# Kernel optimization log

Measured on AMD Instinct MI355X. Metric: run time of the kernel, lower is better.

## Reference

```python
import jax, jax.numpy as jnp
import numpy as np

TEMPERATURE = 0.5
EPS = 1e-12  # matches torch F.normalize clamp_min


def setup_inputs() -> dict:
    key = jax.random.key(0)
    k1, k2 = jax.random.split(key)
    N, D, C = 8192, 128, 64
    out_1 = jax.random.normal(k1, (N, D), dtype=jnp.float32)
    label = jax.random.randint(k2, (N,), 0, C, dtype=jnp.int64)
    return {"out_1": out_1, "label": label}


def reference(out_1, label):
    N = out_1.shape[0]
    # L2 normalize rows (F.normalize with eps clamp)
    norm = jnp.maximum(jnp.linalg.norm(out_1, axis=-1, keepdims=True), EPS)
    x = out_1 / norm
    # exp-scaled cosine similarity matrix [N, N]
    sim = jnp.exp(jnp.matmul(x, x.T) / TEMPERATURE)
    not_diag = 1.0 - jnp.eye(N, dtype=sim.dtype)
    # negatives: all off-diagonal entries per row
    negative_sim = jnp.sum(sim * not_diag, axis=-1)
    # positives: same label, excluding self; mean per row
    pos_mask = (label[:, None] == label[None, :]).astype(sim.dtype) * not_diag
    pos_count = jnp.sum(pos_mask, axis=-1)
    pos_sim = jnp.sum(sim * pos_mask, axis=-1) / pos_count
    return jnp.mean(-jnp.log(pos_sim / negative_sim))
```

## Files before the change

### kernel.cpp

```cpp
#include <hip/hip_runtime.h>
#include <hip/hip_bf16.h>
#include <stdint.h>

typedef __attribute__((ext_vector_type(8))) __bf16 bf16x8;
typedef __attribute__((ext_vector_type(16))) float floatx16;

#if __has_builtin(__builtin_amdgcn_exp2f)
#define EXP2F(x) __builtin_amdgcn_exp2f(x)
#else
#define EXP2F(x) exp2f(x)
#endif

#define GAS __attribute__((address_space(1)))
#define LAS __attribute__((address_space(3)))

#define SCALE_SQRT 1.69864359f

__global__ __launch_bounds__(256) void k_prep(const float* __restrict__ x,
                                              const int* __restrict__ raw,
                                              ushort* __restrict__ xb,
                                              int* __restrict__ lab, int N) {
  const int row = (blockIdx.x * 256 + threadIdx.x) >> 6;
  const int lane = threadIdx.x & 63;
  if (row >= N) return;
  const int probe = raw[2 * lane + 1];
  const bool is64 = (__ballot(probe != 0) == 0ull);
  const float2 v = ((const float2*)(x + (size_t)row * 128))[lane];
  float ss = v.x * v.x + v.y * v.y;
#pragma unroll
  for (int m = 1; m < 64; m <<= 1) ss += __shfl_xor(ss, m, 64);
  const float rn = SCALE_SQRT / fmaxf(sqrtf(ss), 1e-12f);
  __hip_bfloat162 o;
  o.x = __float2bfloat16(v.x * rn);
  o.y = __float2bfloat16(v.y * rn);
  ((__hip_bfloat162*)xb)[row * 64 + lane] = o;
  if (lane == 0) lab[row] = is64 ? raw[2 * row] : raw[row];
}

__global__ __launch_bounds__(256, 2) void k_sim(const ushort* __restrict__ xb,
                                                const int* __restrict__ lab,
                                                float* __restrict__ pneg,
                                                float* __restrict__ ppos,
                                                int N) {
  __shared__ ushort ldsB[128 * 128];
  __shared__ float cb[4 * 2 * 2 * 2 * 32];
  const int tid = threadIdx.x;
  const int lane = tid & 63;
  const int wv = tid >> 6;
  const int l31 = lane & 31, g2 = lane >> 5;
  const int l15 = lane & 15, g4 = lane >> 4;

  const int bid = blockIdx.x;
  int u = (int)((sqrtf(8.0f * (float)bid + 1.0f) - 1.0f) * 0.5f);
  while ((u + 1) * (u + 2) / 2 <= bid) ++u;
  while (u * (u + 1) / 2 > bid) --u;
  const int s = bid - u * (u + 1) / 2;
  const int i0 = s * 128;
  const int jb0 = u * 128;

#pragma unroll
  for (int it = 0; it < 8; ++it) {
    const int r0 = it * 16 + wv * 4;
    const int lr = r0 + g4;
    const int kb = l15 ^ (lr & 15);
    const ushort* gp = xb + (size_t)(jb0 + lr) * 128 + kb * 8;
    __builtin_amdgcn_global_load_lds((GAS void*)gp, (LAS void*)&ldsB[r0 * 128], 16, 0, 0);
  }

  const int arow = i0 + wv * 32 + l31;
  bf16x8 af[8];
#pragma unroll
  for (int kt = 0; kt < 8; ++kt)
    af[kt] = *(const bf16x8*)(xb + (size_t)arow * 128 + (kt * 2 + g2) * 8);

  int liw[4];
#pragma unroll
  for (int q = 0; q < 4; ++q) {
    const int rb = i0 + wv * 32 + 8 * q + 4 * g2;
    liw[q] = (lab[rb] & 255) | ((lab[rb + 1] & 255) << 8) |
             ((lab[rb + 2] & 255) << 16) | ((lab[rb + 3] & 255) << 24);
  }
  int lj[4];
#pragma unroll
  for (int t = 0; t < 2; ++t)
#pragma unroll
    for (int h = 0; h < 2; ++h) lj[t * 2 + h] = lab[jb0 + t * 64 + h * 32 + l31];

  floatx16 vneg = (floatx16)(0.0f), vpos = (floatx16)(0.0f);
  const bool offd = (u != s);
  __syncthreads();

#pragma unroll
  for (int tile = 0; tile < 2; ++tile) {
    floatx16 acc0 = (floatx16)(0.0f), acc1 = (floatx16)(0.0f);
#pragma unroll
    for (int kt = 0; kt < 8; ++kt) {
      const int br0 = tile * 64 + l31;
      const int br1 = tile * 64 + 32 + l31;
      const bf16x8 b0 = *(const bf16x8*)&ldsB[br0 * 128 + (((kt * 2 + g2) ^ (br0 & 15)) * 8)];
      const bf16x8 b1 = *(const bf16x8*)&ldsB[br1 * 128 + (((kt * 2 + g2) ^ (br1 & 15)) * 8)];
      acc0 = __builtin_amdgcn_mfma_f32_32x32x16_bf16(af[kt], b0, acc0, 0, 0, 0);
      acc1 = __builtin_amdgcn_mfma_f32_32x32x16_bf16(af[kt], b1, acc1, 0, 0, 0);
    }

    if (offd) {
      float cn0 = 0.0f, cn1 = 0.0f, cp0 = 0.0f, cp1 = 0.0f;
#pragma unroll
      for (int r = 0; r < 16; ++r) {
        const int lr = (liw[r >> 2] >> ((r & 3) * 8)) & 255;
        const float e0 = EXP2F(acc0[r]);
        const float e1 = EXP2F(acc1[r]);
        const float s0 = (lr == lj[tile * 2 + 0]) ? e0 : 0.0f;
        const float s1 = (lr == lj[tile * 2 + 1]) ? e1 : 0.0f;
        vneg[r] += e0 + e1;
        vpos[r] += s0 + s1;
        cn0 += e0; cp0 += s0;
        cn1 += e1; cp1 += s1;
      }
      {
        float a0 = cn0 + __shfl_xor(cn0, 32, 64);
        float b0 = cp0 + __shfl_xor(cp0, 32, 64);
        float a1 = cn1 + __shfl_xor(cn1, 32, 64);
        float b1 = cp1 + __shfl_xor(cp1, 32, 64);
        if (lane < 32) {
          cb[(((wv * 2 + tile) * 2 + 0) * 2 + 0) * 32 + l31] = a0;
          cb[(((wv * 2 + tile) * 2 + 0) * 2 + 1) * 32 + l31] = b0;
          cb[(((wv * 2 + tile) * 2 + 1) * 2 + 0) * 32 + l31] = a1;
          cb[(((wv * 2 + tile) * 2 + 1) * 2 + 1) * 32 + l31] = b1;
        }
      }
    } else {
      const int jc0 = tile * 64 + l31;
      const int jc1 = tile * 64 + 32 + l31;
#pragma unroll
      for (int r = 0; r < 16; ++r) {
        const int lr = (liw[r >> 2] >> ((r & 3) * 8)) & 255;
        const int ir = wv * 32 + (r & 3) + 8 * (r >> 2) + 4 * g2;
        float e0 = EXP2F(acc0[r]);
        float e1 = EXP2F(acc1[r]);
        if (ir == jc0) e0 = 0.0f;
        if (ir == jc1) e1 = 0.0f;
        vneg[r] += e0 + e1;
        vpos[r] += ((lr == lj[tile * 2 + 0]) ? e0 : 0.0f) +
                   ((lr == lj[tile * 2 + 1]) ? e1 : 0.0f);
      }
    }
  }

#pragma unroll
  for (int r = 0; r < 16; ++r) {
    float n = vneg[r], p = vpos[r];
#pragma unroll
    for (int m = 1; m < 32; m <<= 1) {
      n += __shfl_xor(n, m, 64);
      p += __shfl_xor(p, m, 64);
    }
    if (l31 == 0) {
      const int row = i0 + wv * 32 + (r & 3) + 8 * (r >> 2) + 4 * g2;
      pneg[(size_t)u * N + row] = n;
      ppos[(size_t)u * N + row] = p;
    }
  }

  if (offd) {
    __syncthreads();
    const int c5 = tid & 31;
    const int np = (tid >> 5) & 1;
    const int h = (tid >> 6) & 1;
    const int t = (tid >> 7) & 1;
    float v = 0.0f;
#pragma unroll
    for (int w = 0; w < 4; ++w)
      v += cb[(((w * 2 + t) * 2 + h) * 2 + np) * 32 + c5];
    const int jrow = jb0 + t * 64 + h * 32 + c5;
    if (np == 0) pneg[(size_t)s * N + jrow] = v;
    else         ppos[(size_t)s * N + jrow] = v;
  }
}

__global__ __launch_bounds__(256) void k_final(const float* __restrict__ pneg,
                                               const float* __restrict__ ppos,
                                               const int* __restrict__ lab,
                                               double* __restrict__ partial,
                                               int N, int nstrip) {
  __shared__ int h[64];
  __shared__ double wsum[4];
  const int tid = threadIdx.x;
  if (tid < 64) h[tid] = 0;
  __syncthreads();
  for (int i = tid; i < N; i += 256) atomicAdd(&h[lab[i] & 63], 1);
  __syncthreads();
  const int r = blockIdx.x * 256 + tid;
  double v = 0.0;
  if (r < N) {
    float n = 0.0f, p = 0.0f;
#pragma unroll 8
    for (int cc = 0; cc < nstrip; ++cc) {
      n += pneg[(size_t)cc * N + r];
      p += ppos[(size_t)cc * N + r];
    }
    const float cnt = (float)(h[lab[r] & 63] - 1);
    v = (double)logf(n * cnt / p);
  }
#pragma unroll
  for (int m = 1; m < 64; m <<= 1) v += __shfl_xor(v, m, 64);
  if ((tid & 63) == 0) wsum[tid >> 6] = v;
  __syncthreads();
  if (tid == 0) partial[blockIdx.x] = wsum[0] + wsum[1] + wsum[2] + wsum[3];
}

__global__ __launch_bounds__(64) void k_write(const double* __restrict__ partial,
                                              float* __restrict__ out, int nfb, int N) {
  const int l = threadIdx.x;
  double v = 0.0;
  for (int i = l; i < nfb; i += 64) v += partial[i];
#pragma unroll
  for (int m = 1; m < 64; m <<= 1) v += __shfl_xor(v, m, 64);
  if (l == 0) out[0] = (float)(v / (double)N);
}

extern "C" void kernel_launch(void* const* d_in, const int* in_sizes, int n_in,
                              void* d_out, int out_size, void* d_ws, size_t ws_size,
                              hipStream_t stream) {
  const float* x = (const float*)d_in[0];
  const int* raw_label = (const int*)d_in[1];
  const int N = in_sizes[1];
  const int nstrip = N / 128;
  char* ws = (char*)d_ws;
  ushort* xb = (ushort*)ws;
  float* pneg = (float*)(ws + (size_t)N * 128 * 2);
  float* ppos = pneg + (size_t)nstrip * N;
  int* lab = (int*)(ppos + (size_t)nstrip * N);
  double* partial = (double*)(lab + N);
  float* out = (float*)d_out;

  const int pairs = nstrip * (nstrip + 1) / 2;
  const int nfb = (N + 255) / 256;

  k_prep<<<dim3(N / 4), dim3(256), 0, stream>>>(x, raw_label, xb, lab, N);
  k_sim<<<dim3(pairs), dim3(256), 0, stream>>>(xb, lab, pneg, ppos, N);
  k_final<<<dim3(nfb), dim3(256), 0, stream>>>(pneg, ppos, lab, partial, N, nstrip);
  k_write<<<dim3(1), dim3(64), 0, stream>>>(partial, out, nfb, N);
}
```

Before: 99.65 us.

## Make k_sim persistent over tile pairs with double-buffered LDS prefetch

The similarity kernel now launches a fixed grid of 512 blocks, each walking 4–5 consecutive triangular tile pairs. The next B tile is prefetched into a second LDS buffer while the current one is computed, and column partial sums are deferred into a double-buffered cb array. This hides the global-to-LDS load latency and cuts per-block launch and prologue cost. Labels are stored as bytes and neg/pos partials are packed as float2, which trims memory traffic. The grid size and pair split are hardcoded for N=8192 (2080 pairs = 32*5 + 480*4), and doubling LDS use may limit occupancy.

```diff
diff --git a/kernel.cpp b/kernel.cpp
--- a/kernel.cpp
+++ b/kernel.cpp
@@ -19,7 +19,8 @@
 __global__ __launch_bounds__(256) void k_prep(const float* __restrict__ x,
                                               const int* __restrict__ raw,
                                               ushort* __restrict__ xb,
-                                              int* __restrict__ lab, int N) {
+                                              unsigned char* __restrict__ lab8,
+                                              int N) {
   const int row = (blockIdx.x * 256 + threadIdx.x) >> 6;
   const int lane = threadIdx.x & 63;
   if (row >= N) return;
@@ -34,153 +35,181 @@
   o.x = __float2bfloat16(v.x * rn);
   o.y = __float2bfloat16(v.y * rn);
   ((__hip_bfloat162*)xb)[row * 64 + lane] = o;
-  if (lane == 0) lab[row] = is64 ? raw[2 * row] : raw[row];
+  if (lane == 0) lab8[row] = (unsigned char)(is64 ? raw[2 * row] : raw[row]);
 }
 
 __global__ __launch_bounds__(256, 2) void k_sim(const ushort* __restrict__ xb,
-                                                const int* __restrict__ lab,
-                                                float* __restrict__ pneg,
-                                                float* __restrict__ ppos,
+                                                const unsigned char* __restrict__ lab8,
+                                                float2* __restrict__ ppart,
                                                 int N) {
-  __shared__ ushort ldsB[128 * 128];
-  __shared__ float cb[4 * 2 * 2 * 2 * 32];
+  __shared__ ushort ldsB[2][128 * 128];
+  __shared__ float cb[2][4 * 2 * 2 * 2 * 32];
   const int tid = threadIdx.x;
   const int lane = tid & 63;
   const int wv = tid >> 6;
   const int l31 = lane & 31, g2 = lane >> 5;
   const int l15 = lane & 15, g4 = lane >> 4;
 
-  const int bid = blockIdx.x;
-  int u = (int)((sqrtf(8.0f * (float)bid + 1.0f) - 1.0f) * 0.5f);
-  while ((u + 1) * (u + 2) / 2 <= bid) ++u;
-  while (u * (u + 1) / 2 > bid) --u;
-  const int s = bid - u * (u + 1) / 2;
-  const int i0 = s * 128;
-  const int jb0 = u * 128;
-
-#pragma unroll
-  for (int it = 0; it < 8; ++it) {
-    const int r0 = it * 16 + wv * 4;
-    const int lr = r0 + g4;
-    const int kb = l15 ^ (lr & 15);
-    const ushort* gp = xb + (size_t)(jb0 + lr) * 128 + kb * 8;
-    __builtin_amdgcn_global_load_lds((GAS void*)gp, (LAS void*)&ldsB[r0 * 128], 16, 0, 0);
-  }
-
-  const int arow = i0 + wv * 32 + l31;
-  bf16x8 af[8];
-#pragma unroll
-  for (int kt = 0; kt < 8; ++kt)
-    af[kt] = *(const bf16x8*)(xb + (size_t)arow * 128 + (kt * 2 + g2) * 8);
-
-  int liw[4];
-#pragma unroll
-  for (int q = 0; q < 4; ++q) {
-    const int rb = i0 + wv * 32 + 8 * q + 4 * g2;
-    liw[q] = (lab[rb] & 255) | ((lab[rb + 1] & 255) << 8) |
-             ((lab[rb + 2] & 255) << 16) | ((lab[rb + 3] & 255) << 24);
-  }
-  int lj[4];
-#pragma unroll
-  for (int t = 0; t < 2; ++t)
-#pragma unroll
-    for (int h = 0; h < 2; ++h) lj[t * 2 + h] = lab[jb0 + t * 64 + h * 32 + l31];
-
-  floatx16 vneg = (floatx16)(0.0f), vpos = (floatx16)(0.0f);
-  const bool offd = (u != s);
-  __syncthreads();
-
-#pragma unroll
-  for (int tile = 0; tile < 2; ++tile) {
-    floatx16 acc0 = (floatx16)(0.0f), acc1 = (floatx16)(0.0f);
-#pragma unroll
-    for (int kt = 0; kt < 8; ++kt) {
-      const int br0 = tile * 64 + l31;
-      const int br1 = tile * 64 + 32 + l31;
-      const bf16x8 b0 = *(const bf16x8*)&ldsB[br0 * 128 + (((kt * 2 + g2) ^ (br0 & 15)) * 8)];
-      const bf16x8 b1 = *(const bf16x8*)&ldsB[br1 * 128 + (((kt * 2 + g2) ^ (br1 & 15)) * 8)];
-      acc0 = __builtin_amdgcn_mfma_f32_32x32x16_bf16(af[kt], b0, acc0, 0, 0, 0);
-      acc1 = __builtin_amdgcn_mfma_f32_32x32x16_bf16(af[kt], b1, acc1, 0, 0, 0);
-    }
-
-    if (offd) {
-      float cn0 = 0.0f, cn1 = 0.0f, cp0 = 0.0f, cp1 = 0.0f;
-#pragma unroll
-      for (int r = 0; r < 16; ++r) {
-        const int lr = (liw[r >> 2] >> ((r & 3) * 8)) & 255;
-        const float e0 = EXP2F(acc0[r]);
-        const float e1 = EXP2F(acc1[r]);
-        const float s0 = (lr == lj[tile * 2 + 0]) ? e0 : 0.0f;
-        const float s1 = (lr == lj[tile * 2 + 1]) ? e1 : 0.0f;
-        vneg[r] += e0 + e1;
-        vpos[r] += s0 + s1;
-        cn0 += e0; cp0 += s0;
-        cn1 += e1; cp1 += s1;
-      }
-      {
+  const int b = blockIdx.x;
+  const int p0 = b * 4 + (b < 32 ? b : 32);
+  const int np = (b < 32) ? 5 : 4;
+
+  int u = (int)((sqrtf(8.0f * (float)p0 + 1.0f) - 1.0f) * 0.5f);
+  while ((u + 1) * (u + 2) / 2 <= p0) ++u;
+  while (u * (u + 1) / 2 > p0) --u;
+  int s = p0 - u * (u + 1) / 2;
+
+  auto stageB = [&](int buf, int uu) {
+    const int jb = uu * 128;
+#pragma unroll
+    for (int it = 0; it < 8; ++it) {
+      const int r0 = it * 16 + wv * 4;
+      const int lr = r0 + g4;
+      const int kb = l15 ^ (lr & 15);
+      const ushort* gp = xb + (size_t)(jb + lr) * 128 + kb * 8;
+      __builtin_amdgcn_global_load_lds((GAS void*)gp, (LAS void*)&ldsB[buf][r0 * 128], 16, 0, 0);
+    }
+  };
+
+  stageB(0, u);
+  asm volatile("s_waitcnt vmcnt(0)" ::: "memory");
+  __builtin_amdgcn_s_barrier();
+  __builtin_amdgcn_sched_barrier(0);
+
+  int ps = 0, pu = 0;
+  bool poffd = false;
+  const uint* lab32 = (const uint*)lab8;
+
+  for (int k = 0; k < np; ++k) {
+    const int cur = k & 1;
+    const int i0 = s * 128, jb0 = u * 128;
+    const bool offd = (s != u);
+
+    if (k > 0 && poffd && tid < 128) {
+      const int t = (tid >> 6) & 1, h = (tid >> 5) & 1, c5 = tid & 31;
+      float n = 0.0f, p = 0.0f;
+#pragma unroll
+      for (int w = 0; w < 4; ++w) {
+        n += cb[cur ^ 1][(((w * 2 + t) * 2 + h) * 2 + 0) * 32 + c5];
+        p += cb[cur ^ 1][(((w * 2 + t) * 2 + h) * 2 + 1) * 32 + c5];
+      }
+      const int jrow = pu * 128 + t * 64 + h * 32 + c5;
+      ppart[(size_t)ps * N + jrow] = float2{n, p};
+    }
+
+    const int arow = i0 + wv * 32 + l31;
+    bf16x8 af[8];
+#pragma unroll
+    for (int kt = 0; kt < 8; ++kt)
+      af[kt] = *(const bf16x8*)(xb + (size_t)arow * 128 + (kt * 2 + g2) * 8);
+    uint liw[4];
+#pragma unroll
+    for (int q = 0; q < 4; ++q)
+      liw[q] = lab32[(i0 + wv * 32 + 8 * q + 4 * g2) >> 2];
+    int lj[4];
+#pragma unroll
+    for (int t = 0; t < 2; ++t)
+#pragma unroll
+      for (int h = 0; h < 2; ++h) lj[t * 2 + h] = lab8[jb0 + t * 64 + h * 32 + l31];
+
+    int ns = s + 1, nu = u;
+    if (ns > nu) { ns = 0; ++nu; }
+    if (k + 1 < np) stageB(cur ^ 1, nu);
+
+    floatx16 vneg = (floatx16)(0.0f), vpos = (floatx16)(0.0f);
+#pragma unroll
+    for (int tile = 0; tile < 2; ++tile) {
+      floatx16 acc0 = (floatx16)(0.0f), acc1 = (floatx16)(0.0f);
+#pragma unroll
+      for (int kt = 0; kt < 8; ++kt) {
+        const int br0 = tile * 64 + l31;
+        const int br1 = tile * 64 + 32 + l31;
+        const bf16x8 b0 = *(const bf16x8*)&ldsB[cur][br0 * 128 + (((kt * 2 + g2) ^ (br0 & 15)) * 8)];
+        const bf16x8 b1 = *(const bf16x8*)&ldsB[cur][br1 * 128 + (((kt * 2 + g2) ^ (br1 & 15)) * 8)];
+        acc0 = __builtin_amdgcn_mfma_f32_32x32x16_bf16(af[kt], b0, acc0, 0, 0, 0);
+        acc1 = __builtin_amdgcn_mfma_f32_32x32x16_bf16(af[kt], b1, acc1, 0, 0, 0);
+      }
+      if (offd) {
+        float cn0 = 0.0f, cn1 = 0.0f, cp0 = 0.0f, cp1 = 0.0f;
+#pragma unroll
+        for (int r = 0; r < 16; ++r) {
+          const int lr = (liw[r >> 2] >> ((r & 3) * 8)) & 255;
+          const float e0 = EXP2F(acc0[r]);
+          const float e1 = EXP2F(acc1[r]);
+          const float s0 = (lr == lj[tile * 2 + 0]) ? e0 : 0.0f;
+          const float s1 = (lr == lj[tile * 2 + 1]) ? e1 : 0.0f;
+          vneg[r] += e0 + e1;
+          vpos[r] += s0 + s1;
+          cn0 += e0; cp0 += s0;
+          cn1 += e1; cp1 += s1;
+        }
         float a0 = cn0 + __shfl_xor(cn0, 32, 64);
         float b0 = cp0 + __shfl_xor(cp0, 32, 64);
         float a1 = cn1 + __shfl_xor(cn1, 32, 64);
         float b1 = cp1 + __shfl_xor(cp1, 32, 64);
         if (lane < 32) {
-          cb[(((wv * 2 + tile) * 2 + 0) * 2 + 0) * 32 + l31] = a0;
-          cb[(((wv * 2 + tile) * 2 + 0) * 2 + 1) * 32 + l31] = b0;
-          cb[(((wv * 2 + tile) * 2 + 1) * 2 + 0) * 32 + l31] = a1;
-          cb[(((wv * 2 + tile) * 2 + 1) * 2 + 1) * 32 + l31] = b1;
+          cb[cur][(((wv * 2 + tile) * 2 + 0) * 2 + 0) * 32 + l31] = a0;
+          cb[cur][(((wv * 2 + tile) * 2 + 0) * 2 + 1) * 32 + l31] = b0;
+          cb[cur][(((wv * 2 + tile) * 2 + 1) * 2 + 0) * 32 + l31] = a1;
+          cb[cur][(((wv * 2 + tile) * 2 + 1) * 2 + 1) * 32 + l31] = b1;
         }
-      }
-    } else {
-      const int jc0 = tile * 64 + l31;
-      const int jc1 = tile * 64 + 32 + l31;
-#pragma unroll
-      for (int r = 0; r < 16; ++r) {
-        const int lr = (liw[r >> 2] >> ((r & 3) * 8)) & 255;
-        const int ir = wv * 32 + (r & 3) + 8 * (r >> 2) + 4 * g2;
-        float e0 = EXP2F(acc0[r]);
-        float e1 = EXP2F(acc1[r]);
-        if (ir == jc0) e0 = 0.0f;
-        if (ir == jc1) e1 = 0.0f;
-        vneg[r] += e0 + e1;
-        vpos[r] += ((lr == lj[tile * 2 + 0]) ? e0 : 0.0f) +
-                   ((lr == lj[tile * 2 + 1]) ? e1 : 0.0f);
-      }
-    }
+      } else {
+        const int jc0 = tile * 64 + l31;
+        const int jc1 = tile * 64 + 32 + l31;
+#pragma unroll
+        for (int r = 0; r < 16; ++r) {
+          const int lr = (liw[r >> 2] >> ((r & 3) * 8)) & 255;
+          const int ir = wv * 32 + (r & 3) + 8 * (r >> 2) + 4 * g2;
+          float e0 = EXP2F(acc0[r]);
+          float e1 = EXP2F(acc1[r]);
+          if (ir == jc0) e0 = 0.0f;
+          if (ir == jc1) e1 = 0.0f;
+          vneg[r] += e0 + e1;
+          vpos[r] += ((lr == lj[tile * 2 + 0]) ? e0 : 0.0f) +
+                     ((lr == lj[tile * 2 + 1]) ? e1 : 0.0f);
+        }
+      }
+    }
+
+#pragma unroll
+    for (int r = 0; r < 16; ++r) {
+      float n = vneg[r], p = vpos[r];
+#pragma unroll
+      for (int m = 1; m < 32; m <<= 1) {
+        n += __shfl_xor(n, m, 64);
+        p += __shfl_xor(p, m, 64);
+      }
+      if (l31 == 0) {
+        const int row = i0 + wv * 32 + (r & 3) + 8 * (r >> 2) + 4 * g2;
+        ppart[(size_t)u * N + row] = float2{n, p};
+      }
+    }
+
+    asm volatile("s_waitcnt vmcnt(16) lgkmcnt(0)" ::: "memory");
+    __builtin_amdgcn_s_barrier();
+    __builtin_amdgcn_sched_barrier(0);
+
+    ps = s; pu = u; poffd = offd;
+    s = ns; u = nu;
   }
 
-#pragma unroll
-  for (int r = 0; r < 16; ++r) {
-    float n = vneg[r], p = vpos[r];
-#pragma unroll
-    for (int m = 1; m < 32; m <<= 1) {
-      n += __shfl_xor(n, m, 64);
-      p += __shfl_xor(p, m, 64);
-    }
-    if (l31 == 0) {
-      const int row = i0 + wv * 32 + (r & 3) + 8 * (r >> 2) + 4 * g2;
-      pneg[(size_t)u * N + row] = n;
-      ppos[(size_t)u * N + row] = p;
-    }
+  __syncthreads();
+  if (poffd && tid < 128) {
+    const int last = (np - 1) & 1;
+    const int t = (tid >> 6) & 1, h = (tid >> 5) & 1, c5 = tid & 31;
+    float n = 0.0f, p = 0.0f;
+#pragma unroll
+    for (int w = 0; w < 4; ++w) {
+      n += cb[last][(((w * 2 + t) * 2 + h) * 2 + 0) * 32 + c5];
+      p += cb[last][(((w * 2 + t) * 2 + h) * 2 + 1) * 32 + c5];
+    }
+    const int jrow = pu * 128 + t * 64 + h * 32 + c5;
+    ppart[(size_t)ps * N + jrow] = float2{n, p};
   }
-
-  if (offd) {
-    __syncthreads();
-    const int c5 = tid & 31;
-    const int np = (tid >> 5) & 1;
-    const int h = (tid >> 6) & 1;
-    const int t = (tid >> 7) & 1;
-    float v = 0.0f;
-#pragma unroll
-    for (int w = 0; w < 4; ++w)
-      v += cb[(((w * 2 + t) * 2 + h) * 2 + np) * 32 + c5];
-    const int jrow = jb0 + t * 64 + h * 32 + c5;
-    if (np == 0) pneg[(size_t)s * N + jrow] = v;
-    else         ppos[(size_t)s * N + jrow] = v;
-  }
-}
-
-__global__ __launch_bounds__(256) void k_final(const float* __restrict__ pneg,
-                                               const float* __restrict__ ppos,
-                                               const int* __restrict__ lab,
+}
+
+__global__ __launch_bounds__(256) void k_final(const float2* __restrict__ ppart,
+                                               const unsigned char* __restrict__ lab8,
                                                double* __restrict__ partial,
                                                int N, int nstrip) {
   __shared__ int h[64];
@@ -188,7 +217,7 @@
   const int tid = threadIdx.x;
   if (tid < 64) h[tid] = 0;
   __syncthreads();
-  for (int i = tid; i < N; i += 256) atomicAdd(&h[lab[i] & 63], 1);
+  for (int i = tid; i < N; i += 256) atomicAdd(&h[lab8[i] & 63], 1);
   __syncthreads();
   const int r = blockIdx.x * 256 + tid;
   double v = 0.0;
@@ -196,10 +225,11 @@
     float n = 0.0f, p = 0.0f;
 #pragma unroll 8
     for (int cc = 0; cc < nstrip; ++cc) {
-      n += pneg[(size_t)cc * N + r];
-      p += ppos[(size_t)cc * N + r];
-    }
-    const float cnt = (float)(h[lab[r] & 63] - 1);
+      const float2 w = ppart[(size_t)cc * N + r];
+      n += w.x;
+      p += w.y;
+    }
+    const float cnt = (float)(h[lab8[r] & 63] - 1);
     v = (double)logf(n * cnt / p);
   }
 #pragma unroll
@@ -228,17 +258,15 @@
   const int nstrip = N / 128;
   char* ws = (char*)d_ws;
   ushort* xb = (ushort*)ws;
-  float* pneg = (float*)(ws + (size_t)N * 128 * 2);
-  float* ppos = pneg + (size_t)nstrip * N;
-  int* lab = (int*)(ppos + (size_t)nstrip * N);
-  double* partial = (double*)(lab + N);
+  float2* ppart = (float2*)(ws + (size_t)N * 128 * 2);
+  unsigned char* lab8 = (unsigned char*)(ppart + (size_t)nstrip * N);
+  double* partial = (double*)(lab8 + ((N + 7) & ~7));
   float* out = (float*)d_out;
 
-  const int pairs = nstrip * (nstrip + 1) / 2;
   const int nfb = (N + 255) / 256;
 
-  k_prep<<<dim3(N / 4), dim3(256), 0, stream>>>(x, raw_label, xb, lab, N);
-  k_sim<<<dim3(pairs), dim3(256), 0, stream>>>(xb, lab, pneg, ppos, N);
-  k_final<<<dim3(nfb), dim3(256), 0, stream>>>(pneg, ppos, lab, partial, N, nstrip);
+  k_prep<<<dim3(N / 4), dim3(256), 0, stream>>>(x, raw_label, xb, lab8, N);
+  k_sim<<<dim3(512), dim3(256), 0, stream>>>(xb, lab8, ppart, N);
+  k_final<<<dim3(nfb), dim3(256), 0, stream>>>(ppart, lab8, partial, N, nstrip);
   k_write<<<dim3(1), dim3(64), 0, stream>>>(partial, out, nfb, N);
 }
```

New measurement: 106.7 us. 7.1% more time.

## Load B tiles directly from global, pack labels to bytes and partials to float2

Applied to the files above, without the earlier changes.

Drops the 32 KB LDS staging of the B strip via global_load_lds. Each wave now reads its B fragments straight from global/L2 with a one-step register prefetch, and launch bounds go from 2 to 3 blocks per SM. Labels are stored as bytes so four row labels come in one 32-bit load, and the negative/positive partial sums are interleaved as float2 so each store and each final-pass load is a single vector access. The aim is lower LDS use and more occupancy plus fewer memory transactions. The cost is that all four waves re-read the same B rows from cache instead of sharing them through LDS.

```diff
diff --git a/kernel.cpp b/kernel.cpp
--- a/kernel.cpp
+++ b/kernel.cpp
@@ -11,15 +11,13 @@
 #define EXP2F(x) exp2f(x)
 #endif
 
-#define GAS __attribute__((address_space(1)))
-#define LAS __attribute__((address_space(3)))
-
 #define SCALE_SQRT 1.69864359f
 
 __global__ __launch_bounds__(256) void k_prep(const float* __restrict__ x,
                                               const int* __restrict__ raw,
                                               ushort* __restrict__ xb,
-                                              int* __restrict__ lab, int N) {
+                                              unsigned char* __restrict__ lab8,
+                                              int N) {
   const int row = (blockIdx.x * 256 + threadIdx.x) >> 6;
   const int lane = threadIdx.x & 63;
   if (row >= N) return;
@@ -34,21 +32,18 @@
   o.x = __float2bfloat16(v.x * rn);
   o.y = __float2bfloat16(v.y * rn);
   ((__hip_bfloat162*)xb)[row * 64 + lane] = o;
-  if (lane == 0) lab[row] = is64 ? raw[2 * row] : raw[row];
-}
-
-__global__ __launch_bounds__(256, 2) void k_sim(const ushort* __restrict__ xb,
-                                                const int* __restrict__ lab,
-                                                float* __restrict__ pneg,
-                                                float* __restrict__ ppos,
+  if (lane == 0) lab8[row] = (unsigned char)(is64 ? raw[2 * row] : raw[row]);
+}
+
+__global__ __launch_bounds__(256, 3) void k_sim(const ushort* __restrict__ xb,
+                                                const unsigned char* __restrict__ lab8,
+                                                float2* __restrict__ ppart,
                                                 int N) {
-  __shared__ ushort ldsB[128 * 128];
   __shared__ float cb[4 * 2 * 2 * 2 * 32];
   const int tid = threadIdx.x;
   const int lane = tid & 63;
   const int wv = tid >> 6;
   const int l31 = lane & 31, g2 = lane >> 5;
-  const int l15 = lane & 15, g4 = lane >> 4;
 
   const int bid = blockIdx.x;
   int u = (int)((sqrtf(8.0f * (float)bid + 1.0f) - 1.0f) * 0.5f);
@@ -57,50 +52,46 @@
   const int s = bid - u * (u + 1) / 2;
   const int i0 = s * 128;
   const int jb0 = u * 128;
-
-#pragma unroll
-  for (int it = 0; it < 8; ++it) {
-    const int r0 = it * 16 + wv * 4;
-    const int lr = r0 + g4;
-    const int kb = l15 ^ (lr & 15);
-    const ushort* gp = xb + (size_t)(jb0 + lr) * 128 + kb * 8;
-    __builtin_amdgcn_global_load_lds((GAS void*)gp, (LAS void*)&ldsB[r0 * 128], 16, 0, 0);
-  }
-
-  const int arow = i0 + wv * 32 + l31;
+  const bool offd = (u != s);
+
+  const ushort* arp = xb + (size_t)(i0 + wv * 32 + l31) * 128 + g2 * 8;
   bf16x8 af[8];
 #pragma unroll
-  for (int kt = 0; kt < 8; ++kt)
-    af[kt] = *(const bf16x8*)(xb + (size_t)arow * 128 + (kt * 2 + g2) * 8);
-
-  int liw[4];
-#pragma unroll
-  for (int q = 0; q < 4; ++q) {
-    const int rb = i0 + wv * 32 + 8 * q + 4 * g2;
-    liw[q] = (lab[rb] & 255) | ((lab[rb + 1] & 255) << 8) |
-             ((lab[rb + 2] & 255) << 16) | ((lab[rb + 3] & 255) << 24);
-  }
+  for (int kt = 0; kt < 8; ++kt) af[kt] = *(const bf16x8*)(arp + kt * 16);
+
+  const uint* lab32 = (const uint*)lab8;
+  uint liw[4];
+#pragma unroll
+  for (int q = 0; q < 4; ++q)
+    liw[q] = lab32[(i0 + wv * 32 + 8 * q + 4 * g2) >> 2];
   int lj[4];
 #pragma unroll
   for (int t = 0; t < 2; ++t)
 #pragma unroll
-    for (int h = 0; h < 2; ++h) lj[t * 2 + h] = lab[jb0 + t * 64 + h * 32 + l31];
+    for (int h = 0; h < 2; ++h) lj[t * 2 + h] = lab8[jb0 + t * 64 + h * 32 + l31];
+
+  const ushort* brp = xb + (size_t)(jb0 + l31) * 128 + g2 * 8;
 
   floatx16 vneg = (floatx16)(0.0f), vpos = (floatx16)(0.0f);
-  const bool offd = (u != s);
-  __syncthreads();
-
 #pragma unroll
   for (int tile = 0; tile < 2; ++tile) {
+    const ushort* b0p = brp + (size_t)(tile * 64) * 128;
+    const ushort* b1p = brp + (size_t)(tile * 64 + 32) * 128;
+
     floatx16 acc0 = (floatx16)(0.0f), acc1 = (floatx16)(0.0f);
+    bf16x8 c0 = *(const bf16x8*)(b0p);
+    bf16x8 c1 = *(const bf16x8*)(b1p);
 #pragma unroll
     for (int kt = 0; kt < 8; ++kt) {
-      const int br0 = tile * 64 + l31;
-      const int br1 = tile * 64 + 32 + l31;
-      const bf16x8 b0 = *(const bf16x8*)&ldsB[br0 * 128 + (((kt * 2 + g2) ^ (br0 & 15)) * 8)];
-      const bf16x8 b1 = *(const bf16x8*)&ldsB[br1 * 128 + (((kt * 2 + g2) ^ (br1 & 15)) * 8)];
-      acc0 = __builtin_amdgcn_mfma_f32_32x32x16_bf16(af[kt], b0, acc0, 0, 0, 0);
-      acc1 = __builtin_amdgcn_mfma_f32_32x32x16_bf16(af[kt], b1, acc1, 0, 0, 0);
+      bf16x8 n0 = c0, n1 = c1;
+      if (kt < 7) {
+        n0 = *(const bf16x8*)(b0p + (kt + 1) * 16);
+        n1 = *(const bf16x8*)(b1p + (kt + 1) * 16);
+      }
+      acc0 = __builtin_amdgcn_mfma_f32_32x32x16_bf16(af[kt], c0, acc0, 0, 0, 0);
+      acc1 = __builtin_amdgcn_mfma_f32_32x32x16_bf16(af[kt], c1, acc1, 0, 0, 0);
+      c0 = n0;
+      c1 = n1;
     }
 
     if (offd) {
@@ -117,17 +108,15 @@
         cn0 += e0; cp0 += s0;
         cn1 += e1; cp1 += s1;
       }
-      {
-        float a0 = cn0 + __shfl_xor(cn0, 32, 64);
-        float b0 = cp0 + __shfl_xor(cp0, 32, 64);
-        float a1 = cn1 + __shfl_xor(cn1, 32, 64);
-        float b1 = cp1 + __shfl_xor(cp1, 32, 64);
-        if (lane < 32) {
-          cb[(((wv * 2 + tile) * 2 + 0) * 2 + 0) * 32 + l31] = a0;
-          cb[(((wv * 2 + tile) * 2 + 0) * 2 + 1) * 32 + l31] = b0;
-          cb[(((wv * 2 + tile) * 2 + 1) * 2 + 0) * 32 + l31] = a1;
-          cb[(((wv * 2 + tile) * 2 + 1) * 2 + 1) * 32 + l31] = b1;
-        }
+      float a0 = cn0 + __shfl_xor(cn0, 32, 64);
+      float b0 = cp0 + __shfl_xor(cp0, 32, 64);
+      float a1 = cn1 + __shfl_xor(cn1, 32, 64);
+      float b1 = cp1 + __shfl_xor(cp1, 32, 64);
+      if (lane < 32) {
+        cb[(((wv * 2 + tile) * 2 + 0) * 2 + 0) * 32 + l31] = a0;
+        cb[(((wv * 2 + tile) * 2 + 0) * 2 + 1) * 32 + l31] = b0;
+        cb[(((wv * 2 + tile) * 2 + 1) * 2 + 0) * 32 + l31] = a1;
+        cb[(((wv * 2 + tile) * 2 + 1) * 2 + 1) * 32 + l31] = b1;
       }
     } else {
       const int jc0 = tile * 64 + l31;
@@ -157,30 +146,28 @@
     }
     if (l31 == 0) {
       const int row = i0 + wv * 32 + (r & 3) + 8 * (r >> 2) + 4 * g2;
-      pneg[(size_t)u * N + row] = n;
-      ppos[(size_t)u * N + row] = p;
+      ppart[(size_t)u * N + row] = float2{n, p};
     }
   }
 
   if (offd) {
     __syncthreads();
-    const int c5 = tid & 31;
-    const int np = (tid >> 5) & 1;
-    const int h = (tid >> 6) & 1;
-    const int t = (tid >> 7) & 1;
-    float v = 0.0f;
-#pragma unroll
-    for (int w = 0; w < 4; ++w)
-      v += cb[(((w * 2 + t) * 2 + h) * 2 + np) * 32 + c5];
-    const int jrow = jb0 + t * 64 + h * 32 + c5;
-    if (np == 0) pneg[(size_t)s * N + jrow] = v;
-    else         ppos[(size_t)s * N + jrow] = v;
-  }
-}
-
-__global__ __launch_bounds__(256) void k_final(const float* __restrict__ pneg,
-                                               const float* __restrict__ ppos,
-                                               const int* __restrict__ lab,
+    if (tid < 128) {
+      const int t = (tid >> 6) & 1, h = (tid >> 5) & 1, c5 = tid & 31;
+      float n = 0.0f, p = 0.0f;
+#pragma unroll
+      for (int w = 0; w < 4; ++w) {
+        n += cb[(((w * 2 + t) * 2 + h) * 2 + 0) * 32 + c5];
+        p += cb[(((w * 2 + t) * 2 + h) * 2 + 1) * 32 + c5];
+      }
+      const int jrow = jb0 + t * 64 + h * 32 + c5;
+      ppart[(size_t)s * N + jrow] = float2{n, p};
+    }
+  }
+}
+
+__global__ __launch_bounds__(256) void k_final(const float2* __restrict__ ppart,
+                                               const unsigned char* __restrict__ lab8,
                                                double* __restrict__ partial,
                                                int N, int nstrip) {
   __shared__ int h[64];
@@ -188,7 +175,7 @@
   const int tid = threadIdx.x;
   if (tid < 64) h[tid] = 0;
   __syncthreads();
-  for (int i = tid; i < N; i += 256) atomicAdd(&h[lab[i] & 63], 1);
+  for (int i = tid; i < N; i += 256) atomicAdd(&h[lab8[i] & 63], 1);
   __syncthreads();
   const int r = blockIdx.x * 256 + tid;
   double v = 0.0;
@@ -196,10 +183,11 @@
     float n = 0.0f, p = 0.0f;
 #pragma unroll 8
     for (int cc = 0; cc < nstrip; ++cc) {
-      n += pneg[(size_t)cc * N + r];
-      p += ppos[(size_t)cc * N + r];
-    }
-    const float cnt = (float)(h[lab[r] & 63] - 1);
+      const float2 w = ppart[(size_t)cc * N + r];
+      n += w.x;
+      p += w.y;
+    }
+    const float cnt = (float)(h[lab8[r] & 63] - 1);
     v = (double)logf(n * cnt / p);
   }
 #pragma unroll
@@ -228,17 +216,16 @@
   const int nstrip = N / 128;
   char* ws = (char*)d_ws;
   ushort* xb = (ushort*)ws;
-  float* pneg = (float*)(ws + (size_t)N * 128 * 2);
-  float* ppos = pneg + (size_t)nstrip * N;
-  int* lab = (int*)(ppos + (size_t)nstrip * N);
-  double* partial = (double*)(lab + N);
+  float2* ppart = (float2*)(ws + (size_t)N * 128 * 2);
+  unsigned char* lab8 = (unsigned char*)(ppart + (size_t)nstrip * N);
+  double* partial = (double*)(lab8 + ((N + 7) & ~7));
   float* out = (float*)d_out;
 
   const int pairs = nstrip * (nstrip + 1) / 2;
   const int nfb = (N + 255) / 256;
 
-  k_prep<<<dim3(N / 4), dim3(256), 0, stream>>>(x, raw_label, xb, lab, N);
-  k_sim<<<dim3(pairs), dim3(256), 0, stream>>>(xb, lab, pneg, ppos, N);
-  k_final<<<dim3(nfb), dim3(256), 0, stream>>>(pneg, ppos, lab, partial, N, nstrip);
+  k_prep<<<dim3(N / 4), dim3(256), 0, stream>>>(x, raw_label, xb, lab8, N);
+  k_sim<<<dim3(pairs), dim3(256), 0, stream>>>(xb, lab8, ppart, N);
+  k_final<<<dim3(nfb), dim3(256), 0, stream>>>(ppart, lab8, partial, N, nstrip);
   k_write<<<dim3(1), dim3(64), 0, stream>>>(partial, out, nfb, N);
 }
```

After: 119.0 us. 19.4% more time.
